# Performance work log

Measured on AMD Instinct MI355X. Metric: run time of the kernel, lower is better.

The kernel has to match this reference:

```python
import jax, jax.numpy as jnp
import numpy as np

BETA = 1.0
EPS_MU = 1e-6
EPS_LOG = 1e-8
D_DIM = 2048
M_EVENTS = 16384
T_HORIZON = 100


def setup_inputs() -> dict:
    key = jax.random.key(0)
    k1, k2 = jax.random.split(key)
    # sorted event times in [0, T_HORIZON)
    t_events = jnp.sort(jax.random.uniform(k1, (M_EVENTS,), jnp.float32) * T_HORIZON)
    marks = jax.random.randint(k2, (M_EVENTS,), 0, D_DIM)  # int marks in {0..D-1}
    # learned params, init exactly as in torch module
    log_mu = jnp.full((D_DIM,), -3.0, jnp.float32)
    log_alpha = jnp.full((D_DIM, D_DIM), -4.0, jnp.float32)
    return {
        "t_events": t_events,
        "marks": marks,
        "T_max": T_HORIZON,
        "log_mu": log_mu,
        "log_alpha": log_alpha,
    }


def _loglik(t_events, log_mu, log_alpha, marks, T_max, beta=BETA):
    mu = jax.nn.softplus(log_mu) + EPS_MU          # [D]
    alpha = jax.nn.softplus(log_alpha)             # [D, D]
    D = mu.shape[0]
    # dt[0] = 0 so the first step leaves S (= zeros) untouched, matching the
    # torch loop which skips decay at n == 0.
    dt = jnp.concatenate([jnp.zeros((1,), t_events.dtype), jnp.diff(t_events)])  # [M]

    def step(S, xs):
        dt_n, d = xs
        S = jnp.exp(-beta * dt_n) * S              # exponential decay of state [D]
        lam_d = mu[d] + alpha[d] @ S               # intensity at event's mark
        S = S.at[d].add(1.0)                       # self-excitation bump
        return S, jnp.log(lam_d + EPS_LOG)

    _, log_lams = jax.lax.scan(step, jnp.zeros((D,), mu.dtype), (dt, marks))

    # compensator integral term
    T = jnp.asarray(T_max, t_events.dtype)
    one_minus_exp = 1.0 - jnp.exp(-beta * (T - t_events))          # [M]
    contrib = jax.ops.segment_sum(one_minus_exp, marks, num_segments=D)  # [D]
    integral = mu * T + alpha @ (contrib / beta)                   # [D]
    return log_lams.sum() - integral.sum()


def reference(t_events, marks, T_max, log_mu, log_alpha):
    return _loglik(t_events, log_mu, log_alpha, marks, T_max)
```

## Files before the change

### kernel.cpp

```cpp
#include <hip/hip_runtime.h>
#include <math.h>

#define D_DIM 2048
#define M_EV  16384
#define LCH   32
#define CCH   (M_EV / LCH)
#define SEG   32
#define NSEG  (CCH / SEG)
#define BETA  1.0f

__device__ __forceinline__ float softplus_f(float x){
  float e = __expf(-fabsf(x));
  return fmaxf(x, 0.0f) + __logf(1.0f + e);
}

__device__ __forceinline__ float decode_T(const void* p){
  unsigned bits = *(const unsigned*)p;
  float fv = __uint_as_float(bits);
  return (fv >= 1e-3f && fv <= 1e7f) ? fv : (float)(int)bits;
}

__device__ __forceinline__ float wave_red(float v){
  #pragma unroll
  for (int o = 32; o > 0; o >>= 1) v += __shfl_down(v, o);
  return v;
}

__global__ void k_small(const float* __restrict__ t, const int* __restrict__ m,
                        const void* Tp, const float* __restrict__ log_mu,
                        float* __restrict__ muw, float* __restrict__ contrib,
                        float* __restrict__ SL, float* __restrict__ dchunk,
                        float* __restrict__ cumdec, float* __restrict__ Aseg,
                        float* __restrict__ acc){
  const int b = blockIdx.x, tid = threadIdx.x;
  if (b < 8){
    int j = b*256 + tid;
    float v = softplus_f(log_mu[j]) + 1e-6f;
    muw[j] = v;
    float s = wave_red(v);
    if ((tid & 63) == 0) atomicAdd(&acc[2], s);
  } else if (b < 72){
    int i = (b-8)*256 + tid;
    float T = decode_T(Tp);
    float v = 1.0f - __expf(-BETA * (T - t[i]));
    atomicAdd(&contrib[m[i]], v);
  } else if (b < 136){
    int i = (b-72)*256 + tid;
    int c = i >> 5;
    if (c < CCH - 1){
      float tn = t[(c+1)*LCH];
      float v = __expf(-BETA * (tn - t[i]));
      atomicAdd(&SL[(size_t)c * D_DIM + m[i]], v);
    }
  } else {
    int c = (b-136)*256 + tid;
    float tc = t[c*LCH];
    dchunk[c] = (c < CCH-1) ? __expf(-BETA * (t[(c+1)*LCH] - tc)) : 1.0f;
    int s0c = (c >> 5) << 5;
    cumdec[c] = __expf(-BETA * (tc - t[s0c*LCH]));
    if (b == 136 && tid < NSEG){
      int s = tid;
      Aseg[s] = (s < NSEG-1)
        ? __expf(-BETA * (t[(s+1)*SEG*LCH] - t[s*SEG*LCH])) : 1.0f;
    }
  }
}

__global__ void k_scan_local(float* __restrict__ SL,
                             const float* __restrict__ dchunk,
                             float* __restrict__ Carry){
  const int tid = threadIdx.x;
  const int seg = blockIdx.x >> 3, jb = blockIdx.x & 7;
  const int j = jb*256 + tid;
  const int c0 = seg * SEG;
  const size_t base = (size_t)c0 * D_DIM + j;
  float u = 0.f;
  float cur[4], nxt[4];
  #pragma unroll
  for (int q = 0; q < 4; ++q) cur[q] = SL[base + (size_t)q * D_DIM];
  for (int g = 0; g < SEG; g += 4){
    #pragma unroll
    for (int q = 0; q < 4; ++q)
      nxt[q] = (g+4 < SEG) ? SL[base + (size_t)(g+4+q) * D_DIM] : 0.f;
    #pragma unroll
    for (int q = 0; q < 4; ++q){
      int c = c0 + g + q;
      float l = cur[q];
      SL[(size_t)c * D_DIM + j] = u;
      u = fmaf(dchunk[c], u, l);
    }
    #pragma unroll
    for (int q = 0; q < 4; ++q) cur[q] = nxt[q];
  }
  Carry[(size_t)seg * D_DIM + j] = u;
}

__global__ void k_scan_carry(const float* __restrict__ Carry,
                             const float* __restrict__ Aseg,
                             float* __restrict__ E){
  const int j = blockIdx.x*256 + threadIdx.x;
  float cr[NSEG];
  #pragma unroll
  for (int s = 0; s < NSEG; ++s) cr[s] = Carry[(size_t)s * D_DIM + j];
  float e = 0.f;
  #pragma unroll
  for (int s = 0; s < NSEG; ++s){
    E[(size_t)s * D_DIM + j] = e;
    e = fmaf(Aseg[s], e, cr[s]);
  }
}

__global__ void k_alpha(const float* __restrict__ la,
                        const float* __restrict__ contrib,
                        float* __restrict__ sA, float* __restrict__ acc){
  const int nthreads = gridDim.x * blockDim.x;
  int tid = blockIdx.x * blockDim.x + threadIdx.x;
  const float4* la4 = (const float4*)la;
  float4* sA4 = (float4*)sA;
  float p = 0.f;
  #pragma unroll
  for (int u = 0; u < 8; ++u){
    int i4 = tid + u * nthreads;
    float4 x = la4[i4];
    float4 sp;
    sp.x = softplus_f(x.x); sp.y = softplus_f(x.y);
    sp.z = softplus_f(x.z); sp.w = softplus_f(x.w);
    sA4[i4] = sp;
    int col = (i4 * 4) & (D_DIM - 1);
    p = fmaf(sp.x, contrib[col+0], p);
    p = fmaf(sp.y, contrib[col+1], p);
    p = fmaf(sp.z, contrib[col+2], p);
    p = fmaf(sp.w, contrib[col+3], p);
  }
  __shared__ float red[4];
  float w = wave_red(p);
  int lane = threadIdx.x & 63, wid = threadIdx.x >> 6;
  if (lane == 0) red[wid] = w;
  __syncthreads();
  if (threadIdx.x == 0) atomicAdd(&acc[1], red[0]+red[1]+red[2]+red[3]);
}

__global__ __launch_bounds__(256) void k_events(
    const float* __restrict__ t, const int* __restrict__ m,
    const float* __restrict__ sA, const float* __restrict__ muw,
    const float* __restrict__ SL, const float* __restrict__ E,
    const float* __restrict__ cumdec, float* __restrict__ acc){
  __shared__ float tl[LCH];
  __shared__ int   ml[LCH];
  __shared__ float red[LCH][4];
  const int tid = threadIdx.x;
  const int c = blockIdx.x;
  const int seg = c >> 5;
  const float cd = cumdec[c];

  const float4* sp = (const float4*)(SL + (size_t)c  * D_DIM + tid*8);
  const float4* ep = (const float4*)(E  + (size_t)seg * D_DIM + tid*8);
  float4 s0 = sp[0], s1 = sp[1];
  float4 e0 = ep[0], e1 = ep[1];
  s0.x = fmaf(e0.x, cd, s0.x); s0.y = fmaf(e0.y, cd, s0.y);
  s0.z = fmaf(e0.z, cd, s0.z); s0.w = fmaf(e0.w, cd, s0.w);
  s1.x = fmaf(e1.x, cd, s1.x); s1.y = fmaf(e1.y, cd, s1.y);
  s1.z = fmaf(e1.z, cd, s1.z); s1.w = fmaf(e1.w, cd, s1.w);

  if (tid < LCH){ tl[tid] = t[c*LCH + tid]; ml[tid] = m[c*LCH + tid]; }
  __syncthreads();

  const int lane = tid & 63, wid = tid >> 6;
  const int colb = tid * 8;

  const float* P0 = sA + (size_t)ml[0] * D_DIM + colb;
  float4 a0 = *(const float4*)P0, a1 = *(const float4*)(P0 + 4);
  const float* P1 = sA + (size_t)ml[1] * D_DIM + colb;
  float4 b0 = *(const float4*)P1, b1 = *(const float4*)(P1 + 4);

  #pragma unroll 1
  for (int k = 0; k < LCH; ++k){
    const int d = ml[k];
    const int kn = (k + 2 < LCH) ? k + 2 : LCH - 1;
    const float* Pn = sA + (size_t)ml[kn] * D_DIM + colb;
    float4 c0v = *(const float4*)Pn, c1v = *(const float4*)(Pn + 4);

    const float dec = (k == 0) ? 1.0f : __expf(-BETA * (tl[k] - tl[k-1]));
    s0.x *= dec; s0.y *= dec; s0.z *= dec; s0.w *= dec;
    s1.x *= dec; s1.y *= dec; s1.z *= dec; s1.w *= dec;

    float p = 0.f;
    p = fmaf(a0.x, s0.x, p); p = fmaf(a0.y, s0.y, p);
    p = fmaf(a0.z, s0.z, p); p = fmaf(a0.w, s0.w, p);
    p = fmaf(a1.x, s1.x, p); p = fmaf(a1.y, s1.y, p);
    p = fmaf(a1.z, s1.z, p); p = fmaf(a1.w, s1.w, p);

    if ((d >> 3) == tid){
      int r = d & 7;
      s0.x += (r==0) ? 1.f : 0.f; s0.y += (r==1) ? 1.f : 0.f;
      s0.z += (r==2) ? 1.f : 0.f; s0.w += (r==3) ? 1.f : 0.f;
      s1.x += (r==4) ? 1.f : 0.f; s1.y += (r==5) ? 1.f : 0.f;
      s1.z += (r==6) ? 1.f : 0.f; s1.w += (r==7) ? 1.f : 0.f;
    }

    float w = wave_red(p);
    if (lane == 0) red[k][wid] = w;

    a0 = b0; a1 = b1; b0 = c0v; b1 = c1v;
  }

  __syncthreads();
  float lg = 0.f;
  if (tid < LCH){
    float lam = muw[ml[tid]] + red[tid][0] + red[tid][1]
                             + red[tid][2] + red[tid][3];
    lg = __logf(lam + 1e-8f);
  }
  if (tid < 64){
    float w = wave_red(lg);
    if (tid == 0) atomicAdd(&acc[0], w);
  }
}

__global__ void k_final(const float* __restrict__ acc, const void* Tp,
                        float* __restrict__ out){
  float T = decode_T(Tp);
  out[0] = acc[0] - (T * acc[2] + acc[1] * (1.0f / BETA));
}

extern "C" void kernel_launch(void* const* d_in, const int* in_sizes, int n_in,
                              void* d_out, int out_size, void* d_ws, size_t ws_size,
                              hipStream_t stream) {
  const float* t_events  = (const float*)d_in[0];
  const int*   marks     = (const int*)  d_in[1];
  const void*  Tp        =               d_in[2];
  const float* log_mu    = (const float*)d_in[3];
  const float* log_alpha = (const float*)d_in[4];
  float* out = (float*)d_out;

  float* ws      = (float*)d_ws;
  float* SL      = ws;
  float* contrib = SL + (size_t)CCH * D_DIM;
  float* acc     = contrib + D_DIM;
  float* Carry   = acc + 16;
  float* E       = Carry + (size_t)NSEG * D_DIM;
  float* muw     = E + (size_t)NSEG * D_DIM;
  float* dchunk  = muw + D_DIM;
  float* cumdec  = dchunk + CCH;
  float* Aseg    = cumdec + CCH;
  float* sA      = Aseg + NSEG;

  size_t zero_floats = (size_t)CCH * D_DIM + D_DIM + 16;
  hipMemsetAsync(d_ws, 0, zero_floats * sizeof(float), stream);

  k_small     <<<138, 256, 0, stream>>>(t_events, marks, Tp, log_mu, muw,
                                        contrib, SL, dchunk, cumdec, Aseg, acc);
  k_scan_local<<<NSEG*8, 256, 0, stream>>>(SL, dchunk, Carry);
  k_scan_carry<<<8, 256, 0, stream>>>(Carry, Aseg, E);
  k_alpha     <<<512, 256, 0, stream>>>(log_alpha, contrib, sA, acc);
  k_events    <<<CCH, 256, 0, stream>>>(t_events, marks, sA, muw,
                                        SL, E, cumdec, acc);
  k_final     <<<1, 1, 0, stream>>>(acc, Tp, out);
}
```

Baseline: 120.1 us.

## Store softplus(alpha) as bf16 and widen event blocks to 512 threads

k_alpha now writes the softplus'd alpha matrix as bf16, with round-to-nearest-even, instead of fp32. This halves the bytes of the row gathers in k_events. k_events moves to 512 threads with 4 columns each, precomputes the per-event decay factors in shared memory, and prefetches 4 rows ahead with a manually unrolled loop. The bf16 storage adds rounding error to the per-event intensities, and the wider blocks mean more waves per reduction.

```diff
diff --git a/kernel.cpp b/kernel.cpp
--- a/kernel.cpp
+++ b/kernel.cpp
@@ -12,6 +12,14 @@
 __device__ __forceinline__ float softplus_f(float x){
   float e = __expf(-fabsf(x));
   return fmaxf(x, 0.0f) + __logf(1.0f + e);
+}
+
+__device__ __forceinline__ unsigned short f2bf(float f){
+  unsigned b = __float_as_uint(f);
+  return (unsigned short)((b + 0x7FFFu + ((b >> 16) & 1u)) >> 16);
+}
+__device__ __forceinline__ float bf2f(unsigned short u){
+  return __uint_as_float(((unsigned)u) << 16);
 }
 
 __device__ __forceinline__ float decode_T(const void* p){
@@ -112,11 +120,12 @@
 
 __global__ void k_alpha(const float* __restrict__ la,
                         const float* __restrict__ contrib,
-                        float* __restrict__ sA, float* __restrict__ acc){
+                        unsigned short* __restrict__ sA,
+                        float* __restrict__ acc){
   const int nthreads = gridDim.x * blockDim.x;
   int tid = blockIdx.x * blockDim.x + threadIdx.x;
   const float4* la4 = (const float4*)la;
-  float4* sA4 = (float4*)sA;
+  ushort4* sA4 = (ushort4*)sA;
   float p = 0.f;
   #pragma unroll
   for (int u = 0; u < 8; ++u){
@@ -125,7 +134,9 @@
     float4 sp;
     sp.x = softplus_f(x.x); sp.y = softplus_f(x.y);
     sp.z = softplus_f(x.z); sp.w = softplus_f(x.w);
-    sA4[i4] = sp;
+    ushort4 h;
+    h.x = f2bf(sp.x); h.y = f2bf(sp.y); h.z = f2bf(sp.z); h.w = f2bf(sp.w);
+    sA4[i4] = h;
     int col = (i4 * 4) & (D_DIM - 1);
     p = fmaf(sp.x, contrib[col+0], p);
     p = fmaf(sp.y, contrib[col+1], p);
@@ -140,75 +151,74 @@
   if (threadIdx.x == 0) atomicAdd(&acc[1], red[0]+red[1]+red[2]+red[3]);
 }
 
-__global__ __launch_bounds__(256) void k_events(
+__global__ __launch_bounds__(512) void k_events(
     const float* __restrict__ t, const int* __restrict__ m,
-    const float* __restrict__ sA, const float* __restrict__ muw,
+    const unsigned short* __restrict__ sA, const float* __restrict__ muw,
     const float* __restrict__ SL, const float* __restrict__ E,
     const float* __restrict__ cumdec, float* __restrict__ acc){
-  __shared__ float tl[LCH];
   __shared__ int   ml[LCH];
-  __shared__ float red[LCH][4];
+  __shared__ float decs[LCH];
+  __shared__ float red[LCH][8];
   const int tid = threadIdx.x;
   const int c = blockIdx.x;
   const int seg = c >> 5;
   const float cd = cumdec[c];
 
-  const float4* sp = (const float4*)(SL + (size_t)c  * D_DIM + tid*8);
-  const float4* ep = (const float4*)(E  + (size_t)seg * D_DIM + tid*8);
-  float4 s0 = sp[0], s1 = sp[1];
-  float4 e0 = ep[0], e1 = ep[1];
-  s0.x = fmaf(e0.x, cd, s0.x); s0.y = fmaf(e0.y, cd, s0.y);
-  s0.z = fmaf(e0.z, cd, s0.z); s0.w = fmaf(e0.w, cd, s0.w);
-  s1.x = fmaf(e1.x, cd, s1.x); s1.y = fmaf(e1.y, cd, s1.y);
-  s1.z = fmaf(e1.z, cd, s1.z); s1.w = fmaf(e1.w, cd, s1.w);
-
-  if (tid < LCH){ tl[tid] = t[c*LCH + tid]; ml[tid] = m[c*LCH + tid]; }
+  const float4 sv = *(const float4*)(SL + (size_t)c  * D_DIM + tid*4);
+  const float4 ev = *(const float4*)(E  + (size_t)seg * D_DIM + tid*4);
+  float4 s;
+  s.x = fmaf(ev.x, cd, sv.x); s.y = fmaf(ev.y, cd, sv.y);
+  s.z = fmaf(ev.z, cd, sv.z); s.w = fmaf(ev.w, cd, sv.w);
+
+  if (tid < LCH){
+    ml[tid] = m[c*LCH + tid];
+    float tk = t[c*LCH + tid];
+    float tp = (tid == 0) ? tk : t[c*LCH + tid - 1];
+    decs[tid] = __expf(-BETA * (tk - tp));
+  }
   __syncthreads();
 
   const int lane = tid & 63, wid = tid >> 6;
-  const int colb = tid * 8;
-
-  const float* P0 = sA + (size_t)ml[0] * D_DIM + colb;
-  float4 a0 = *(const float4*)P0, a1 = *(const float4*)(P0 + 4);
-  const float* P1 = sA + (size_t)ml[1] * D_DIM + colb;
-  float4 b0 = *(const float4*)P1, b1 = *(const float4*)(P1 + 4);
-
-  #pragma unroll 1
-  for (int k = 0; k < LCH; ++k){
-    const int d = ml[k];
-    const int kn = (k + 2 < LCH) ? k + 2 : LCH - 1;
-    const float* Pn = sA + (size_t)ml[kn] * D_DIM + colb;
-    float4 c0v = *(const float4*)Pn, c1v = *(const float4*)(Pn + 4);
-
-    const float dec = (k == 0) ? 1.0f : __expf(-BETA * (tl[k] - tl[k-1]));
-    s0.x *= dec; s0.y *= dec; s0.z *= dec; s0.w *= dec;
-    s1.x *= dec; s1.y *= dec; s1.z *= dec; s1.w *= dec;
-
-    float p = 0.f;
-    p = fmaf(a0.x, s0.x, p); p = fmaf(a0.y, s0.y, p);
-    p = fmaf(a0.z, s0.z, p); p = fmaf(a0.w, s0.w, p);
-    p = fmaf(a1.x, s1.x, p); p = fmaf(a1.y, s1.y, p);
-    p = fmaf(a1.z, s1.z, p); p = fmaf(a1.w, s1.w, p);
-
-    if ((d >> 3) == tid){
-      int r = d & 7;
-      s0.x += (r==0) ? 1.f : 0.f; s0.y += (r==1) ? 1.f : 0.f;
-      s0.z += (r==2) ? 1.f : 0.f; s0.w += (r==3) ? 1.f : 0.f;
-      s1.x += (r==4) ? 1.f : 0.f; s1.y += (r==5) ? 1.f : 0.f;
-      s1.z += (r==6) ? 1.f : 0.f; s1.w += (r==7) ? 1.f : 0.f;
-    }
-
-    float w = wave_red(p);
-    if (lane == 0) red[k][wid] = w;
-
-    a0 = b0; a1 = b1; b0 = c0v; b1 = c1v;
-  }
+  const int colb = tid * 4;
+
+  ushort4 pf0 = *(const ushort4*)(sA + (size_t)ml[0] * D_DIM + colb);
+  ushort4 pf1 = *(const ushort4*)(sA + (size_t)ml[1] * D_DIM + colb);
+  ushort4 pf2 = *(const ushort4*)(sA + (size_t)ml[2] * D_DIM + colb);
+  ushort4 pf3 = *(const ushort4*)(sA + (size_t)ml[3] * D_DIM + colb);
+
+#define STAGE(Q) {                                                          \
+    const int kk = k + (Q);                                                 \
+    const int d = ml[kk];                                                   \
+    const int kn = (kk + 4 < LCH) ? kk + 4 : LCH - 1;                       \
+    ushort4 nx = *(const ushort4*)(sA + (size_t)ml[kn] * D_DIM + colb);     \
+    const float dec = decs[kk];                                             \
+    s.x *= dec; s.y *= dec; s.z *= dec; s.w *= dec;                         \
+    float p = 0.f;                                                          \
+    p = fmaf(bf2f(pf##Q.x), s.x, p);                                        \
+    p = fmaf(bf2f(pf##Q.y), s.y, p);                                        \
+    p = fmaf(bf2f(pf##Q.z), s.z, p);                                        \
+    p = fmaf(bf2f(pf##Q.w), s.w, p);                                        \
+    if ((d >> 2) == tid){                                                   \
+      int r = d & 3;                                                        \
+      s.x += (r==0) ? 1.f : 0.f; s.y += (r==1) ? 1.f : 0.f;                 \
+      s.z += (r==2) ? 1.f : 0.f; s.w += (r==3) ? 1.f : 0.f;                 \
+    }                                                                       \
+    float w = wave_red(p);                                                  \
+    if (lane == 0) red[kk][wid] = w;                                        \
+    pf##Q = nx;                                                             \
+  }
+
+  for (int k = 0; k < LCH; k += 4){
+    STAGE(0) STAGE(1) STAGE(2) STAGE(3)
+  }
+#undef STAGE
 
   __syncthreads();
   float lg = 0.f;
   if (tid < LCH){
-    float lam = muw[ml[tid]] + red[tid][0] + red[tid][1]
-                             + red[tid][2] + red[tid][3];
+    const float* r = red[tid];
+    float lam = muw[ml[tid]] + ((r[0]+r[1])+(r[2]+r[3]))
+                             + ((r[4]+r[5])+(r[6]+r[7]));
     lg = __logf(lam + 1e-8f);
   }
   if (tid < 64){
@@ -243,7 +253,7 @@
   float* dchunk  = muw + D_DIM;
   float* cumdec  = dchunk + CCH;
   float* Aseg    = cumdec + CCH;
-  float* sA      = Aseg + NSEG;
+  unsigned short* sA = (unsigned short*)(Aseg + NSEG);
 
   size_t zero_floats = (size_t)CCH * D_DIM + D_DIM + 16;
   hipMemsetAsync(d_ws, 0, zero_floats * sizeof(float), stream);
@@ -253,7 +263,7 @@
   k_scan_local<<<NSEG*8, 256, 0, stream>>>(SL, dchunk, Carry);
   k_scan_carry<<<8, 256, 0, stream>>>(Carry, Aseg, E);
   k_alpha     <<<512, 256, 0, stream>>>(log_alpha, contrib, sA, acc);
-  k_events    <<<CCH, 256, 0, stream>>>(t_events, marks, sA, muw,
+  k_events    <<<CCH, 512, 0, stream>>>(t_events, marks, sA, muw,
                                         SL, E, cumdec, acc);
   k_final     <<<1, 1, 0, stream>>>(acc, Tp, out);
 }
```

New measurement: 116.7 us. 1.03x faster.
